# Performance work log

Hardware: AMD Instinct MI355X
Metric: run time of the kernel (lower is better)

The kernel has to match this reference:

```python
import jax, jax.numpy as jnp
import numpy as np

BOX_LOWER, BOX_UPPER = -3.0, 3.0
EPS = 1e-7


def base_quartic_spline(t):
    # Piecewise quartic B-spline-like basis on |t| with breakpoints 0.5, 1.5, 2.5.
    ta = jnp.abs(t)
    # branch 0: |t| < 0.5
    z0 = ta + 0.5
    r0 = (11.0 + z0 * (12.0 + z0 * (-6.0 + z0 * (-12.0 + 6.0 * z0)))) / 24.0
    # branch 1: 0.5 <= |t| < 1.5
    z1 = 1.5 - ta
    r1 = (1.0 + z1 * (4.0 + z1 * (6.0 + z1 * (4.0 - 4.0 * z1)))) / 24.0
    # branch 2: 1.5 <= |t| < 2.5
    z2 = (2.5 - ta) * (2.5 - ta)
    r2 = z2 * z2 / 24.0
    out = jnp.where(ta >= 0.5, r1, r0)
    out = jnp.where(ta >= 1.5, r2, out)
    return jnp.where(ta >= 2.5, jnp.zeros_like(ta), out)


def setup_inputs() -> dict:
    key = jax.random.key(0)
    k1, k2 = jax.random.split(key)
    b, f, n, h, w = 16, 16, 64, 64, 64
    x = jax.random.normal(k1, (b, f, h, w), dtype=jnp.float32)
    weight_tensor = jax.random.uniform(k2, (f, n), dtype=jnp.float32)
    nodes = jnp.linspace(BOX_LOWER, BOX_UPPER, n, dtype=jnp.float32)
    return {"x": x, "weight_tensor": weight_tensor, "nodes": nodes}


def reference(x, weight_tensor, nodes):
    n = nodes.shape[0]
    scale = (BOX_UPPER - BOX_LOWER) / (n - 1)
    # (b, f, n, h, w) broadcasted scaled distance to nodes
    t = (x[:, :, None, :, :] - nodes.reshape(1, 1, n, 1, 1)) / scale
    basis = base_quartic_spline(t)
    y = jnp.einsum('bfnhw,fn->bfhw', basis, jnp.exp(weight_tensor))
    return jnp.sum(jnp.log(y + EPS))
```

## Files before the change

### kernel.cpp

```cpp
#include <hip/hip_runtime.h>

constexpr int B_ = 16, F_ = 16, N_ = 64, H_ = 64, W_ = 64;
constexpr int TOTAL = B_ * F_ * H_ * W_;
constexpr float LOWER = -3.0f, UPPER = 3.0f;
constexpr int THREADS = 256;
constexpr int BLOCKS  = 256;
constexpr int VEC = TOTAL / 4;
constexpr int PER_THREAD = VEC / (THREADS * BLOCKS);

__global__ __launch_bounds__(THREADS) void quartic_spline_logsum(
    const float* __restrict__ x,
    const float* __restrict__ weight,
    float* __restrict__ out)
{
    __shared__ float ew[F_ * N_];
    const int tid = threadIdx.x;
    for (int i = tid; i < F_ * N_; i += THREADS) ew[i] = __expf(weight[i]);
    __syncthreads();

    const float inv_scale = (float)(N_ - 1) / (UPPER - LOWER);

    float local = 0.0f;
    int idx4 = blockIdx.x * THREADS + tid;

    #pragma unroll
    for (int it = 0; it < PER_THREAD; ++it, idx4 += THREADS * BLOCKS) {
        const float4 v = reinterpret_cast<const float4*>(x)[idx4];
        const float* __restrict__ ewf = &ew[((idx4 >> 10) & (F_ - 1)) * N_];

        const float vals[4] = {v.x, v.y, v.z, v.w};
        #pragma unroll
        for (int j = 0; j < 4; ++j) {
            const float xv = vals[j];
            const float u = (xv - LOWER) * inv_scale;
            const int kf = (int)floorf(u);
            float y = 0.0f;
            #pragma unroll
            for (int d = 0; d < 6; ++d) {
                const int n = kf - 2 + d;
                const float t  = u - (float)n;
                const float ta = fabsf(t);
                const float z0 = ta + 0.5f;
                const float r0 = 11.0f + z0 * (12.0f + z0 * (-6.0f + z0 * (-12.0f + 6.0f * z0)));
                const float z1 = 1.5f - ta;
                const float r1 = 1.0f + z1 * (4.0f + z1 * (6.0f + z1 * (4.0f - 4.0f * z1)));
                const float z2 = 2.5f - ta;
                const float z2s = z2 * z2;
                const float r2 = z2s * z2s;
                float r = ta < 0.5f ? r0 : (ta < 1.5f ? r1 : r2);
                r = (ta < 2.5f) ? r : 0.0f;
                const bool valid = ((unsigned)n < (unsigned)N_);
                const int nc = valid ? n : 0;
                r = valid ? r : 0.0f;
                y += r * ewf[nc];
            }
            local += __logf(y * (1.0f / 24.0f) + 1e-7f);
        }
    }

    #pragma unroll
    for (int off = 32; off > 0; off >>= 1)
        local += __shfl_down(local, off, 64);

    __shared__ float wpart[THREADS / 64];
    if ((tid & 63) == 0) wpart[tid >> 6] = local;
    __syncthreads();
    if (tid == 0) {
        float s = wpart[0] + wpart[1] + wpart[2] + wpart[3];
        atomicAdd(out, s);
    }
}

extern "C" void kernel_launch(void* const* d_in, const int* in_sizes, int n_in,
                              void* d_out, int out_size, void* d_ws, size_t ws_size,
                              hipStream_t stream) {
    const float* x      = (const float*)d_in[0];
    const float* weight = (const float*)d_in[1];
    float* out = (float*)d_out;

    hipMemsetAsync(out, 0, sizeof(float), stream);

    quartic_spline_logsum<<<BLOCKS, THREADS, 0, stream>>>(x, weight, out);
}
```

Measured before the change: 73.84 us.

## Use closed-form 5-tap centered quartic weights and two-stage block reduction

Each sample's 6-tap evaluation, with branchy piecewise polynomials, is replaced by 5 branch-free closed-form quartic B-spline weights computed around the rounded grid position. The launch becomes 256 blocks of 1024 threads, each handling one float4. The memset plus atomicAdd is replaced by per-block partials in workspace and a second single-block reduction kernel. The aim is to cut ALU work per element and avoid atomics, at the cost of an extra kernel launch and a wider block.

```diff
diff --git a/kernel.cpp b/kernel.cpp
--- a/kernel.cpp
+++ b/kernel.cpp
@@ -1,61 +1,54 @@
 #include <hip/hip_runtime.h>
 
-constexpr int B_ = 16, F_ = 16, N_ = 64, H_ = 64, W_ = 64;
-constexpr int TOTAL = B_ * F_ * H_ * W_;
+constexpr int F_ = 16, N_ = 64;
+constexpr int TOTAL = 16 * 16 * 64 * 64;
+constexpr int VEC = TOTAL / 4;
+constexpr int THREADS = 1024;
+constexpr int BLOCKS = VEC / THREADS;
 constexpr float LOWER = -3.0f, UPPER = 3.0f;
-constexpr int THREADS = 256;
-constexpr int BLOCKS  = 256;
-constexpr int VEC = TOTAL / 4;
-constexpr int PER_THREAD = VEC / (THREADS * BLOCKS);
 
-__global__ __launch_bounds__(THREADS) void quartic_spline_logsum(
+__global__ __launch_bounds__(THREADS) void spline_partial(
     const float* __restrict__ x,
     const float* __restrict__ weight,
-    float* __restrict__ out)
+    float* __restrict__ partials)
 {
     __shared__ float ew[F_ * N_];
     const int tid = threadIdx.x;
-    for (int i = tid; i < F_ * N_; i += THREADS) ew[i] = __expf(weight[i]);
+    ew[tid] = __expf(weight[tid]);
     __syncthreads();
 
-    const float inv_scale = (float)(N_ - 1) / (UPPER - LOWER);
+    const int idx4 = blockIdx.x * THREADS + tid;
+    const float4 v = reinterpret_cast<const float4*>(x)[idx4];
+    const float* __restrict__ ewf = &ew[(blockIdx.x & (F_ - 1)) * N_];
 
+    const float vals[4] = {v.x, v.y, v.z, v.w};
     float local = 0.0f;
-    int idx4 = blockIdx.x * THREADS + tid;
 
     #pragma unroll
-    for (int it = 0; it < PER_THREAD; ++it, idx4 += THREADS * BLOCKS) {
-        const float4 v = reinterpret_cast<const float4*>(x)[idx4];
-        const float* __restrict__ ewf = &ew[((idx4 >> 10) & (F_ - 1)) * N_];
+    for (int j = 0; j < 4; ++j) {
+        const float u = fmaf(vals[j], 10.5f, 31.5f);
+        const float r = rintf(u);
+        const float s = u - r;
+        const int n0 = (int)r - 2;
 
-        const float vals[4] = {v.x, v.y, v.z, v.w};
+        const float p = 0.5f - s, q = 0.5f + s;
+        const float p2 = p * p, q2 = q * q, s2 = s * s;
+        float w[5];
+        w[0] = p2 * p2;
+        w[1] = 1.0f + p * (4.0f + p * (6.0f + p * (4.0f - 4.0f * p)));
+        w[2] = fmaf(s2, fmaf(s2, 6.0f, -15.0f), 14.375f);
+        w[3] = 1.0f + q * (4.0f + q * (6.0f + q * (4.0f - 4.0f * q)));
+        w[4] = q2 * q2;
+
+        float y = 0.0f;
         #pragma unroll
-        for (int j = 0; j < 4; ++j) {
-            const float xv = vals[j];
-            const float u = (xv - LOWER) * inv_scale;
-            const int kf = (int)floorf(u);
-            float y = 0.0f;
-            #pragma unroll
-            for (int d = 0; d < 6; ++d) {
-                const int n = kf - 2 + d;
-                const float t  = u - (float)n;
-                const float ta = fabsf(t);
-                const float z0 = ta + 0.5f;
-                const float r0 = 11.0f + z0 * (12.0f + z0 * (-6.0f + z0 * (-12.0f + 6.0f * z0)));
-                const float z1 = 1.5f - ta;
-                const float r1 = 1.0f + z1 * (4.0f + z1 * (6.0f + z1 * (4.0f - 4.0f * z1)));
-                const float z2 = 2.5f - ta;
-                const float z2s = z2 * z2;
-                const float r2 = z2s * z2s;
-                float r = ta < 0.5f ? r0 : (ta < 1.5f ? r1 : r2);
-                r = (ta < 2.5f) ? r : 0.0f;
-                const bool valid = ((unsigned)n < (unsigned)N_);
-                const int nc = valid ? n : 0;
-                r = valid ? r : 0.0f;
-                y += r * ewf[nc];
-            }
-            local += __logf(y * (1.0f / 24.0f) + 1e-7f);
+        for (int d = 0; d < 5; ++d) {
+            const int n = n0 + d;
+            const bool valid = ((unsigned)n < (unsigned)N_);
+            const float wd = valid ? w[d] : 0.0f;
+            y += wd * ewf[valid ? n : 0];
         }
+        local += __logf(fmaf(y, 1.0f / 24.0f, 1e-7f));
     }
 
     #pragma unroll
@@ -66,9 +59,25 @@
     if ((tid & 63) == 0) wpart[tid >> 6] = local;
     __syncthreads();
     if (tid == 0) {
-        float s = wpart[0] + wpart[1] + wpart[2] + wpart[3];
-        atomicAdd(out, s);
+        float s = 0.0f;
+        #pragma unroll
+        for (int i = 0; i < THREADS / 64; ++i) s += wpart[i];
+        partials[blockIdx.x] = s;
     }
+}
+
+__global__ __launch_bounds__(256) void reduce_partials(
+    const float* __restrict__ partials, float* __restrict__ out)
+{
+    const int tid = threadIdx.x;
+    float v = partials[tid];
+    #pragma unroll
+    for (int off = 32; off > 0; off >>= 1)
+        v += __shfl_down(v, off, 64);
+    __shared__ float wpart[4];
+    if ((tid & 63) == 0) wpart[tid >> 6] = v;
+    __syncthreads();
+    if (tid == 0) out[0] = wpart[0] + wpart[1] + wpart[2] + wpart[3];
 }
 
 extern "C" void kernel_launch(void* const* d_in, const int* in_sizes, int n_in,
@@ -76,9 +85,9 @@
                               hipStream_t stream) {
     const float* x      = (const float*)d_in[0];
     const float* weight = (const float*)d_in[1];
-    float* out = (float*)d_out;
+    float* out      = (float*)d_out;
+    float* partials = (float*)d_ws;
 
-    hipMemsetAsync(out, 0, sizeof(float), stream);
-
-    quartic_spline_logsum<<<BLOCKS, THREADS, 0, stream>>>(x, weight, out);
+    spline_partial<<<BLOCKS, THREADS, 0, stream>>>(x, weight, partials);
+    reduce_partials<<<1, 256, 0, stream>>>(partials, out);
 }
```

New measurement: 60.39 us. -18.2%, faster.
